# Kernel tuning notes

Measured on AMD Instinct MI355X. Metric: run time of the kernel, lower is better.

The kernel has to match this reference:

```python
import jax, jax.numpy as jnp
import numpy as np

N_NODES = 100000
N_EDGES = 1600000
N_GRAPHS = 256
IN_C = 64
HID = 128
OUT = 128
BN_EPS = 1e-5


def setup_inputs() -> dict:
    key = jax.random.key(0)
    ks = jax.random.split(key, 24)
    x = jax.random.normal(ks[0], (N_NODES, IN_C), jnp.float32)
    edge_index = jax.random.randint(ks[1], (2, N_EDGES), 0, N_NODES, dtype=jnp.int64 if jax.config.jax_enable_x64 else jnp.int32)
    batch = jnp.sort(jax.random.randint(ks[2], (N_NODES,), 0, N_GRAPHS))

    def lin(k, i, o):
        return (jax.random.normal(k, (i, o), jnp.float32) / np.float32(np.sqrt(i)))

    d = {"x": x, "edge_index": edge_index, "batch": batch}
    in_dims = [IN_C, HID, HID]
    for l in range(3):
        d[f"w1_{l}"] = lin(ks[3 + 6 * l], in_dims[l], HID)
        d[f"b1_{l}"] = jnp.zeros((HID,), jnp.float32)
        d[f"w2_{l}"] = lin(ks[4 + 6 * l], HID, HID)
        d[f"b2_{l}"] = jnp.zeros((HID,), jnp.float32)
        d[f"gamma_{l}"] = jnp.ones((HID,), jnp.float32)
        d[f"beta_{l}"] = jnp.zeros((HID,), jnp.float32)
    d["proj_w"] = lin(ks[22], HID, OUT)
    d["proj_b"] = jnp.zeros((OUT,), jnp.float32)
    return d


def _gin_forward(x, edge_index, batch, layers, proj_w, proj_b):
    src, dst = edge_index[0], edge_index[1]
    h = x
    for (w1, b1, w2, b2, g, b) in layers:
        # GINConv (eps=0, aggr='add'): MLP(h_i + sum_{j->i} h_j)
        agg = jax.ops.segment_sum(h[src], dst, num_segments=h.shape[0])
        z = h + agg
        z = jax.nn.relu(z @ w1 + b1) @ w2 + b2
        # BatchNorm1d, training mode (biased batch stats)
        mean = z.mean(axis=0)
        var = z.var(axis=0)
        z = (z - mean) * jax.lax.rsqrt(var + BN_EPS) * g + b
        h = jax.nn.relu(z)
    # global_mean_pool over graph ids
    s = jax.ops.segment_sum(h, batch, num_segments=N_GRAPHS)
    cnt = jax.ops.segment_sum(jnp.ones((h.shape[0], 1), h.dtype), batch, num_segments=N_GRAPHS)
    hg = s / jnp.maximum(cnt, 1.0)
    return hg @ proj_w + proj_b


def reference(x, edge_index, batch,
              w1_0, b1_0, w2_0, b2_0, gamma_0, beta_0,
              w1_1, b1_1, w2_1, b2_1, gamma_1, beta_1,
              w1_2, b1_2, w2_2, b2_2, gamma_2, beta_2,
              proj_w, proj_b):
    layers = [
        (w1_0, b1_0, w2_0, b2_0, gamma_0, beta_0),
        (w1_1, b1_1, w2_1, b2_1, gamma_1, beta_1),
        (w1_2, b1_2, w2_2, b2_2, gamma_2, beta_2),
    ]
    return _gin_forward(x, edge_index, batch, layers, proj_w, proj_b)
```

## Files before the change

kernel.cpp:

```cpp
#include <hip/hip_runtime.h>

#define N_NODES 100000
#define N_EDGES 1600000
#define N_GRAPHS 256
#define HID 128
#define BN_EPS 1e-5f

#define NT 1563
#define EB 4096
#define RB 391
#define MBLK 391
#define PB 3128

typedef __bf16 bf16x8 __attribute__((ext_vector_type(8)));
typedef __bf16 bf16x4 __attribute__((ext_vector_type(4)));
typedef __bf16 bf16x2 __attribute__((ext_vector_type(2)));
typedef float f32x4 __attribute__((ext_vector_type(4)));

__global__ __launch_bounds__(256) void setup_kernel(
    const float* __restrict__ x, __bf16* __restrict__ xb,
    const float* __restrict__ wa, const float* __restrict__ wb,
    const float* __restrict__ wc, const float* __restrict__ wd,
    const float* __restrict__ we, const float* __restrict__ wf,
    __bf16* __restrict__ wt,
    const int* __restrict__ batch, int* __restrict__ counts,
    const int* __restrict__ ei, int* __restrict__ tcnt) {
  __shared__ int hist[NT];
  int b = blockIdx.x;
  if (b < 6250) {
    int idx = b * 256 + threadIdx.x;
    if (idx >= N_NODES * 16) return;
    f32x4 v = ((const f32x4*)x)[idx];
    bf16x4 o = {(__bf16)v[0], (__bf16)v[1], (__bf16)v[2], (__bf16)v[3]};
    ((bf16x4*)xb)[idx] = o;
  } else if (b < 6250 + 352) {
    int idx = (b - 6250) * 256 + threadIdx.x;
    if (idx >= 90112) return;
    const float* w;
    int K, local;
    if (idx < 8192) { w = wa; K = 64; local = idx; }
    else {
      int s = (idx - 8192) / 16384;
      local = (idx - 8192) - s * 16384;
      K = 128;
      w = (s == 0) ? wb : (s == 1) ? wc : (s == 2) ? wd : (s == 3) ? we : wf;
    }
    int n = local / K, k = local - n * K;
    wt[idx] = (__bf16)w[k * 128 + n];
  } else if (b < 6609) {
    int t = (b - 6602) * 256 + threadIdx.x;
    int r0 = t * 64;
    if (r0 >= N_NODES) return;
    int rend = min(r0 + 64, N_NODES);
    int curg = batch[r0], cnt = 0;
    for (int r = r0; r < rend; r++) {
      int g = batch[r];
      if (g != curg) {
        atomicAdd(&counts[curg], cnt);
        curg = g;
        cnt = 1;
      } else {
        cnt++;
      }
    }
    atomicAdd(&counts[curg], cnt);
  } else {
    int t = threadIdx.x;
    for (int i = t; i < NT; i += 256) hist[i] = 0;
    __syncthreads();
    int base = (b - 6609) * EB;
#pragma unroll 4
    for (int i = 0; i < EB / 256; i++) {
      int e = base + i * 256 + t;
      if (e < N_EDGES) atomicAdd(&hist[ei[N_EDGES + e] >> 6], 1);
    }
    __syncthreads();
    for (int i = t; i < NT; i += 256) {
      int h = hist[i];
      if (h) atomicAdd(&tcnt[i], h);
    }
  }
}

__global__ __launch_bounds__(256) void tile_scan_kernel(const int* __restrict__ tcnt,
                                                        int* __restrict__ tstart,
                                                        int* __restrict__ gcursor) {
  __shared__ int ps[256];
  int t = threadIdx.x;
  const int CH = (NT + 255) / 256;
  int lo = t * CH, hi = min(lo + CH, NT);
  int s = 0;
  for (int i = lo; i < hi; i++) s += tcnt[i];
  ps[t] = s;
  __syncthreads();
  for (int off = 1; off < 256; off <<= 1) {
    int v = ps[t];
    int u = (t >= off) ? ps[t - off] : 0;
    __syncthreads();
    ps[t] = v + u;
    __syncthreads();
  }
  int base = (t == 0) ? 0 : ps[t - 1];
  for (int i = lo; i < hi; i++) {
    tstart[i] = base;
    gcursor[i] = base;
    base += tcnt[i];
  }
  if (t == 0) tstart[NT] = N_EDGES;
}

__global__ __launch_bounds__(256) void reorder2_kernel(const int* __restrict__ ei,
                                                       int* __restrict__ gcursor,
                                                       int* __restrict__ epack) {
  __shared__ int hist[NT];
  int t = threadIdx.x;
  for (int i = t; i < NT; i += 256) hist[i] = 0;
  __syncthreads();
  int base = blockIdx.x * EB;
#pragma unroll 4
  for (int i = 0; i < EB / 256; i++) {
    int e = base + i * 256 + t;
    if (e < N_EDGES) atomicAdd(&hist[ei[N_EDGES + e] >> 6], 1);
  }
  __syncthreads();
  for (int i = t; i < NT; i += 256) {
    int h = hist[i];
    if (h) hist[i] = atomicAdd(&gcursor[i], h);
  }
  __syncthreads();
#pragma unroll 4
  for (int i = 0; i < EB / 256; i++) {
    int e = base + i * 256 + t;
    if (e < N_EDGES) {
      int d = ei[N_EDGES + e];
      int s = ei[e];
      int pos = atomicAdd(&hist[d >> 6], 1);
      epack[pos] = (s << 6) | (d & 63);
    }
  }
}

__global__ __launch_bounds__(256) void row_sort_kernel(const int* __restrict__ tstart,
                                                       const int* __restrict__ epack,
                                                       int* __restrict__ starts,
                                                       int* __restrict__ srcs) {
  __shared__ int cnt[64];
  __shared__ int rbase[65];
  __shared__ int rofs[64];
  int t = threadIdx.x, b = blockIdx.x;
  int ts = tstart[b], te = tstart[b + 1];
  if (t < 64) cnt[t] = 0;
  __syncthreads();
  for (int i = ts + t; i < te; i += 256) atomicAdd(&cnt[epack[i] & 63], 1);
  __syncthreads();
  if (t == 0) {
    int a = 0;
    for (int r = 0; r < 64; r++) { rbase[r] = a; a += cnt[r]; }
    rbase[64] = a;
  }
  __syncthreads();
  if (t < 64) rofs[t] = ts + rbase[t];
  if (t <= 64) {
    int gr = b * 64 + t;
    if (gr <= N_NODES) starts[gr] = ts + rbase[t];
  }
  __syncthreads();
  for (int i = ts + t; i < te; i += 256) {
    int p = epack[i];
    int pos = atomicAdd(&rofs[p & 63], 1);
    srcs[pos] = p >> 6;
  }
}

template <int C, bool BN>
__global__ __launch_bounds__(256) void gather_kernel(const __bf16* __restrict__ h,
                                                     const float* __restrict__ accum,
                                                     const float* __restrict__ gamma,
                                                     const float* __restrict__ beta,
                                                     const int* __restrict__ starts,
                                                     const int* __restrict__ srcs,
                                                     __bf16* __restrict__ z) {
  const int lane = threadIdx.x & 63;
  const int row = __builtin_amdgcn_readfirstlane(blockIdx.x * 4 + (threadIdx.x >> 6));
  const int e0 = starts[row], e1 = starts[row + 1];

  if constexpr (C == 128) {
    float a0 = 0.f, a1 = 0.f, b0 = 0.f, b1 = 0.f;
    if constexpr (BN) {
      const int c0 = lane * 2, c1 = c0 + 1;
      const float invN = 1.f / (float)N_NODES;
      float m0 = accum[c0] * invN, m1 = accum[c1] * invN;
      float v0 = accum[HID + c0] * invN - m0 * m0;
      float v1 = accum[HID + c1] * invN - m1 * m1;
      a0 = gamma[c0] * rsqrtf(v0 + BN_EPS);
      a1 = gamma[c1] * rsqrtf(v1 + BN_EPS);
      b0 = beta[c0] - m0 * a0;
      b1 = beta[c1] - m1 * a1;
    }
#define ACCBN(vv, ss)                                                  \
    do {                                                               \
      if constexpr (BN) {                                              \
        ss.x += fmaxf(fmaf(a0, (float)(vv)[0], b0), 0.f);              \
        ss.y += fmaxf(fmaf(a1, (float)(vv)[1], b1), 0.f);              \
      } else {                                                         \
        ss.x += (float)(vv)[0];                                        \
        ss.y += (float)(vv)[1];                                        \
      }                                                                \
    } while (0)
    float2 s0 = {0.f, 0.f}, s1 = {0.f, 0.f}, s2 = {0.f, 0.f}, s3 = {0.f, 0.f};
    float2 s4 = {0.f, 0.f}, s5 = {0.f, 0.f}, s6 = {0.f, 0.f}, s7 = {0.f, 0.f};
    int e = e0;
    for (; e + 7 < e1; e += 8) {
      int i0 = srcs[e];
      int i1 = srcs[e + 1];
      int i2 = srcs[e + 2];
      int i3 = srcs[e + 3];
      int i4 = srcs[e + 4];
      int i5 = srcs[e + 5];
      int i6 = srcs[e + 6];
      int i7 = srcs[e + 7];
      bf16x2 v0 = *(const bf16x2*)(h + (size_t)i0 * 128 + lane * 2);
      bf16x2 v1 = *(const bf16x2*)(h + (size_t)i1 * 128 + lane * 2);
      bf16x2 v2 = *(const bf16x2*)(h + (size_t)i2 * 128 + lane * 2);
      bf16x2 v3 = *(const bf16x2*)(h + (size_t)i3 * 128 + lane * 2);
      bf16x2 v4 = *(const bf16x2*)(h + (size_t)i4 * 128 + lane * 2);
      bf16x2 v5 = *(const bf16x2*)(h + (size_t)i5 * 128 + lane * 2);
      bf16x2 v6 = *(const bf16x2*)(h + (size_t)i6 * 128 + lane * 2);
      bf16x2 v7 = *(const bf16x2*)(h + (size_t)i7 * 128 + lane * 2);
      ACCBN(v0, s0);
      ACCBN(v1, s1);
      ACCBN(v2, s2);
      ACCBN(v3, s3);
      ACCBN(v4, s4);
      ACCBN(v5, s5);
      ACCBN(v6, s6);
      ACCBN(v7, s7);
    }
    for (; e + 3 < e1; e += 4) {
      int i0 = srcs[e];
      int i1 = srcs[e + 1];
      int i2 = srcs[e + 2];
      int i3 = srcs[e + 3];
      bf16x2 v0 = *(const bf16x2*)(h + (size_t)i0 * 128 + lane * 2);
      bf16x2 v1 = *(const bf16x2*)(h + (size_t)i1 * 128 + lane * 2);
      bf16x2 v2 = *(const bf16x2*)(h + (size_t)i2 * 128 + lane * 2);
      bf16x2 v3 = *(const bf16x2*)(h + (size_t)i3 * 128 + lane * 2);
      ACCBN(v0, s0);
      ACCBN(v1, s1);
      ACCBN(v2, s2);
      ACCBN(v3, s3);
    }
    for (; e < e1; e++) {
      int i0 = srcs[e];
      bf16x2 vv = *(const bf16x2*)(h + (size_t)i0 * 128 + lane * 2);
      ACCBN(vv, s0);
    }
    bf16x2 sv = *(const bf16x2*)(h + (size_t)row * 128 + lane * 2);
    ACCBN(sv, s0);
    float tx = ((s0.x + s1.x) + (s2.x + s3.x)) + ((s4.x + s5.x) + (s6.x + s7.x));
    float ty = ((s0.y + s1.y) + (s2.y + s3.y)) + ((s4.y + s5.y) + (s6.y + s7.y));
    bf16x2 o = {(__bf16)tx, (__bf16)ty};
    *(bf16x2*)(z + (size_t)row * 128 + lane * 2) = o;
#undef ACCBN
  } else {
    float s0 = 0.f, s1 = 0.f, s2 = 0.f, s3 = 0.f;
    float s4 = 0.f, s5 = 0.f, s6 = 0.f, s7 = 0.f;
    int e = e0;
    for (; e + 7 < e1; e += 8) {
      int i0 = srcs[e];
      int i1 = srcs[e + 1];
      int i2 = srcs[e + 2];
      int i3 = srcs[e + 3];
      int i4 = srcs[e + 4];
      int i5 = srcs[e + 5];
      int i6 = srcs[e + 6];
      int i7 = srcs[e + 7];
      s0 += (float)h[(size_t)i0 * 64 + lane];
      s1 += (float)h[(size_t)i1 * 64 + lane];
      s2 += (float)h[(size_t)i2 * 64 + lane];
      s3 += (float)h[(size_t)i3 * 64 + lane];
      s4 += (float)h[(size_t)i4 * 64 + lane];
      s5 += (float)h[(size_t)i5 * 64 + lane];
      s6 += (float)h[(size_t)i6 * 64 + lane];
      s7 += (float)h[(size_t)i7 * 64 + lane];
    }
    for (; e + 3 < e1; e += 4) {
      int i0 = srcs[e];
      int i1 = srcs[e + 1];
      int i2 = srcs[e + 2];
      int i3 = srcs[e + 3];
      s0 += (float)h[(size_t)i0 * 64 + lane];
      s1 += (float)h[(size_t)i1 * 64 + lane];
      s2 += (float)h[(size_t)i2 * 64 + lane];
      s3 += (float)h[(size_t)i3 * 64 + lane];
    }
    for (; e < e1; e++) {
      int i0 = srcs[e];
      s0 += (float)h[(size_t)i0 * 64 + lane];
    }
    s0 += (float)h[(size_t)row * 64 + lane];
    float tot = ((s0 + s1) + (s2 + s3)) + ((s4 + s5) + (s6 + s7));
    z[(size_t)row * 64 + lane] = (__bf16)tot;
  }
}

template <int CIN>
__global__ __launch_bounds__(512, 1) void mlp_kernel(
    const __bf16* __restrict__ z, const __bf16* __restrict__ w1t,
    const float* __restrict__ b1, const __bf16* __restrict__ w2t,
    const float* __restrict__ b2, __bf16* __restrict__ u,
    float* __restrict__ part) {
  constexpr int CINP = CIN + 8;
  constexpr int TS = HID + 8;
  __shared__ __align__(16) __bf16 w1s[128 * CINP];
  __shared__ __align__(16) __bf16 w2s[128 * TS];
  __shared__ __align__(16) __bf16 hsm[8 * 16 * TS];

  const int tid = threadIdx.x;

  for (int i = tid; i < 128 * (CIN / 8); i += 512) {
    int r = i / (CIN / 8), c = i - r * (CIN / 8);
    *(bf16x8*)(w1s + r * CINP + c * 8) = *(const bf16x8*)(w1t + r * CIN + c * 8);
  }
  for (int i = tid; i < 128 * 16; i += 512) {
    int r = i >> 4, c = i & 15;
    *(bf16x8*)(w2s + r * TS + c * 8) = *(const bf16x8*)(w2t + r * HID + c * 8);
  }
  __syncthreads();

  const int wid = tid >> 6;
  const int lane = tid & 63;
  const int l16 = lane & 15;
  const int quad = lane >> 4;
  const int wgid = blockIdx.x * 8 + wid;
  const int rowbase = wgid * 32;
  const int nvalid = min(32, N_NODES - rowbase);
  __bf16* sm = hsm + wid * 16 * TS;

  if (nvalid <= 0) {
    float2 z2 = {0.f, 0.f};
    *(float2*)(part + (size_t)wgid * 256 + lane * 2) = z2;
    *(float2*)(part + (size_t)wgid * 256 + HID + lane * 2) = z2;
    return;
  }

  const f32x4 zero4 = {0.f, 0.f, 0.f, 0.f};
  float s0 = 0.f, q0 = 0.f, s1 = 0.f, q1 = 0.f;

#pragma unroll
  for (int m = 0; m < 2; m++) {
    const int mbase = rowbase + m * 16;
    const int nv_m = min(16, max(0, nvalid - m * 16));

    f32x4 acc[8];
#pragma unroll
    for (int ct = 0; ct < 8; ct++) acc[ct] = zero4;
#pragma unroll
    for (int ks = 0; ks < CIN / 32; ks++) {
      bf16x8 af = *(const bf16x8*)(z + (size_t)min(mbase + l16, N_NODES - 1) * CIN +
                                   ks * 32 + quad * 8);
#pragma unroll
      for (int ct = 0; ct < 8; ct++) {
        bf16x8 bfr = *(const bf16x8*)(w1s + (ct * 16 + l16) * CINP + ks * 32 + quad * 8);
        acc[ct] = __builtin_amdgcn_mfma_f32_16x16x32_bf16(af, bfr, acc[ct], 0, 0, 0);
      }
    }
#pragma unroll
    for (int ct = 0; ct < 8; ct++) {
      int col = ct * 16 + l16;
      float bias = b1[col];
#pragma unroll
      for (int r = 0; r < 4; r++) {
        float v = acc[ct][r] + bias;
        sm[(quad * 4 + r) * TS + col] = (__bf16)(v > 0.f ? v : 0.f);
      }
    }

#pragma unroll
    for (int ct = 0; ct < 8; ct++) acc[ct] = zero4;
#pragma unroll
    for (int ks = 0; ks < HID / 32; ks++) {
      bf16x8 af = *(const bf16x8*)(sm + l16 * TS + ks * 32 + quad * 8);
#pragma unroll
      for (int ct = 0; ct < 8; ct++) {
        bf16x8 bfr = *(const bf16x8*)(w2s + (ct * 16 + l16) * TS + ks * 32 + quad * 8);
        acc[ct] = __builtin_amdgcn_mfma_f32_16x16x32_bf16(af, bfr, acc[ct], 0, 0, 0);
      }
    }

#pragma unroll
    for (int ct = 0; ct < 8; ct++) {
      int col = ct * 16 + l16;
      float bias = b2[col];
#pragma unroll
      for (int r = 0; r < 4; r++)
        sm[(quad * 4 + r) * TS + col] = (__bf16)(acc[ct][r] + bias);
    }

    for (int f = lane; f < nv_m * 16; f += 64) {
      int r = f >> 4, c8 = f & 15;
      bf16x8 v = *(const bf16x8*)(sm + r * TS + c8 * 8);
      *(bf16x8*)(u + (size_t)(mbase + r) * HID + c8 * 8) = v;
    }

    for (int r = 0; r < nv_m; r++) {
      bf16x2 v = *(const bf16x2*)(sm + r * TS + lane * 2);
      float f0 = (float)v[0], f1 = (float)v[1];
      s0 += f0; q0 += f0 * f0;
      s1 += f1; q1 += f1 * f1;
    }
  }

  {
    float2 sp = {s0, s1}, qp = {q0, q1};
    *(float2*)(part + (size_t)wgid * 256 + lane * 2) = sp;
    *(float2*)(part + (size_t)wgid * 256 + HID + lane * 2) = qp;
  }
}

__global__ __launch_bounds__(256) void reduce_part_kernel(const float* __restrict__ part,
                                                          float* __restrict__ accum) {
  int t = threadIdx.x;
  float s = 0.f;
  for (int r = blockIdx.x; r < PB; r += gridDim.x)
    s += part[(size_t)r * 256 + t];
  atomicAdd(&accum[t], s);
}

__global__ __launch_bounds__(128) void bn_apply_pool_kernel(const __bf16* __restrict__ u,
                                                            const float* __restrict__ accum,
                                                            const float* __restrict__ gamma,
                                                            const float* __restrict__ beta,
                                                            const int* __restrict__ batch,
                                                            float* __restrict__ pool) {
  int c = threadIdx.x;
  int r0 = blockIdx.x * 64;
  if (r0 >= N_NODES) return;
  int rend = min(r0 + 64, N_NODES);
  const float invN = 1.f / (float)N_NODES;
  float mean = accum[c] * invN;
  float var = accum[HID + c] * invN - mean * mean;
  float a = gamma[c] * rsqrtf(var + BN_EPS);
  float b = beta[c] - mean * a;
  float accv = 0.f;
  int curg = -1;
  for (int r = r0; r < rend; r++) {
    int g = batch[r];
    if (g != curg) {
      if (curg >= 0) atomicAdd(&pool[curg * HID + c], accv);
      curg = g;
      accv = 0.f;
    }
    float v = (float)u[(size_t)r * HID + c];
    v = v * a + b;
    accv += (v > 0.f ? v : 0.f);
  }
  if (curg >= 0) atomicAdd(&pool[curg * HID + c], accv);
}

__global__ __launch_bounds__(128) void pool_proj_kernel(const float* __restrict__ pool,
                                                        const int* __restrict__ counts,
                                                        const float* __restrict__ pw,
                                                        const float* __restrict__ pb,
                                                        float* __restrict__ out) {
  int g = blockIdx.x;
  int c = threadIdx.x;
  __shared__ float hg[HID];
  float cnt = (float)max(counts[g], 1);
  hg[c] = pool[g * HID + c] / cnt;
  __syncthreads();
  float acc = pb[c];
#pragma unroll 8
  for (int k = 0; k < HID; k++) acc += hg[k] * pw[k * HID + c];
  out[g * HID + c] = acc;
}

extern "C" void kernel_launch(void* const* d_in, const int* in_sizes, int n_in,
                              void* d_out, int out_size, void* d_ws, size_t ws_size,
                              hipStream_t stream) {
  (void)in_sizes; (void)n_in; (void)out_size; (void)ws_size;
  const float* x = (const float*)d_in[0];
  const int* ei = (const int*)d_in[1];
  const int* batch = (const int*)d_in[2];
  const float* w1[3] = {(const float*)d_in[3], (const float*)d_in[9], (const float*)d_in[15]};
  const float* b1[3] = {(const float*)d_in[4], (const float*)d_in[10], (const float*)d_in[16]};
  const float* w2[3] = {(const float*)d_in[5], (const float*)d_in[11], (const float*)d_in[17]};
  const float* b2[3] = {(const float*)d_in[6], (const float*)d_in[12], (const float*)d_in[18]};
  const float* gm[3] = {(const float*)d_in[7], (const float*)d_in[13], (const float*)d_in[19]};
  const float* bt[3] = {(const float*)d_in[8], (const float*)d_in[14], (const float*)d_in[20]};
  const float* pw = (const float*)d_in[21];
  const float* pb = (const float*)d_in[22];
  float* out = (float*)d_out;

  char* ws = (char*)d_ws;
  __bf16* bufA = (__bf16*)ws;        ws += (size_t)N_NODES * HID * 2;
  __bf16* bufB = (__bf16*)ws;        ws += (size_t)N_NODES * HID * 2;
  __bf16* bufC = (__bf16*)ws;        ws += (size_t)N_NODES * HID * 2;
  __bf16* z0 = (__bf16*)ws;          ws += (size_t)N_NODES * 64 * 2;
  __bf16* xb = (__bf16*)ws;          ws += (size_t)N_NODES * 64 * 2;
  int* srcs = (int*)ws;              ws += (size_t)N_EDGES * 4;
  int* epack = (int*)ws;             ws += (size_t)N_EDGES * 4;
  int* starts = (int*)ws;            ws += (size_t)(N_NODES + 1) * 4;
  int* tcnt = (int*)ws;              ws += NT * 4;
  int* tstart = (int*)ws;            ws += (NT + 1) * 4;
  int* gcursor = (int*)ws;           ws += NT * 4;
  ws = (char*)(((uintptr_t)ws + 63) & ~(uintptr_t)63);
  float* part = (float*)ws;          ws += (size_t)PB * 256 * 4;
  __bf16* wt_all = (__bf16*)ws;      ws += 90112 * 2;
  ws = (char*)(((uintptr_t)ws + 63) & ~(uintptr_t)63);
  float* accum = (float*)ws;         ws += 3 * 256 * 4;
  float* pool = (float*)ws;          ws += N_GRAPHS * HID * 4;
  int* counts = (int*)ws;            ws += N_GRAPHS * 4;

  __bf16* w1t0 = wt_all;
  __bf16* w2t0 = wt_all + 8192;
  __bf16* w1t1 = wt_all + 24576;
  __bf16* w2t1 = wt_all + 40960;
  __bf16* w1t2 = wt_all + 57344;
  __bf16* w2t2 = wt_all + 73728;

  float* acc0 = accum;
  float* acc1 = accum + 256;
  float* acc2 = accum + 512;

  const int gat_blocks = (N_NODES + 3) / 4;

  hipMemsetAsync(accum, 0, 3 * 256 * 4 + (size_t)N_GRAPHS * HID * 4 + N_GRAPHS * 4, stream);
  hipMemsetAsync(tcnt, 0, NT * 4, stream);

  setup_kernel<<<7000, 256, 0, stream>>>(x, xb, w1[0], w2[0], w1[1], w2[1],
                                         w1[2], w2[2], wt_all, batch, counts, ei, tcnt);

  tile_scan_kernel<<<1, 256, 0, stream>>>(tcnt, tstart, gcursor);
  reorder2_kernel<<<RB, 256, 0, stream>>>(ei, gcursor, epack);
  row_sort_kernel<<<NT, 256, 0, stream>>>(tstart, epack, starts, srcs);

  gather_kernel<64, false><<<gat_blocks, 256, 0, stream>>>(xb, nullptr, nullptr, nullptr,
                                                           starts, srcs, z0);
  mlp_kernel<64><<<MBLK, 512, 0, stream>>>(z0, w1t0, b1[0], w2t0, b2[0], bufA, part);
  reduce_part_kernel<<<128, 256, 0, stream>>>(part, acc0);

  gather_kernel<128, true><<<gat_blocks, 256, 0, stream>>>(bufA, acc0, gm[0], bt[0],
                                                           starts, srcs, bufC);
  mlp_kernel<128><<<MBLK, 512, 0, stream>>>(bufC, w1t1, b1[1], w2t1, b2[1], bufB, part);
  reduce_part_kernel<<<128, 256, 0, stream>>>(part, acc1);

  gather_kernel<128, true><<<gat_blocks, 256, 0, stream>>>(bufB, acc1, gm[1], bt[1],
                                                           starts, srcs, bufC);
  mlp_kernel<128><<<MBLK, 512, 0, stream>>>(bufC, w1t2, b1[2], w2t2, b2[2], bufA, part);
  reduce_part_kernel<<<128, 256, 0, stream>>>(part, acc2);

  bn_apply_pool_kernel<<<NT, 128, 0, stream>>>(bufA, acc2, gm[2], bt[2], batch, pool);

  pool_proj_kernel<<<N_GRAPHS, 128, 0, stream>>>(pool, counts, pw, pb, out);
}
```

Measured before the change: 490.7 us.

## Split fused MLP kernel into two GEMM kernels with intermediate buffer

Replaces the fused two-layer MLP kernel (512 threads, one block per CU, large LDS) with two separate kernels: gemm1 writes the ReLU hidden activations to a global buffer and gemm2 reads them back, applies bias and computes BN partial statistics in registers with shuffle reductions. Each kernel uses smaller blocks with less LDS to raise occupancy. In exchange it adds an extra global write and read of a 100000x128 bf16 tensor per layer and an extra launch per layer. Row bounds checks are dropped because NW*32 exactly equals N_NODES.

```diff
diff --git a/kernel.cpp b/kernel.cpp
--- a/kernel.cpp
+++ b/kernel.cpp
@@ -9,7 +9,8 @@
 #define NT 1563
 #define EB 4096
 #define RB 391
-#define MBLK 391
+#define GB 782
+#define NW 3125
 #define PB 3128
 
 typedef __bf16 bf16x8 __attribute__((ext_vector_type(8)));
@@ -305,26 +306,16 @@
 }
 
 template <int CIN>
-__global__ __launch_bounds__(512, 1) void mlp_kernel(
+__global__ __launch_bounds__(256, 4) void gemm1_kernel(
     const __bf16* __restrict__ z, const __bf16* __restrict__ w1t,
-    const float* __restrict__ b1, const __bf16* __restrict__ w2t,
-    const float* __restrict__ b2, __bf16* __restrict__ u,
-    float* __restrict__ part) {
+    const float* __restrict__ b1, __bf16* __restrict__ t) {
   constexpr int CINP = CIN + 8;
-  constexpr int TS = HID + 8;
   __shared__ __align__(16) __bf16 w1s[128 * CINP];
-  __shared__ __align__(16) __bf16 w2s[128 * TS];
-  __shared__ __align__(16) __bf16 hsm[8 * 16 * TS];
 
   const int tid = threadIdx.x;
-
-  for (int i = tid; i < 128 * (CIN / 8); i += 512) {
+  for (int i = tid; i < 128 * (CIN / 8); i += 256) {
     int r = i / (CIN / 8), c = i - r * (CIN / 8);
     *(bf16x8*)(w1s + r * CINP + c * 8) = *(const bf16x8*)(w1t + r * CIN + c * 8);
-  }
-  for (int i = tid; i < 128 * 16; i += 512) {
-    int r = i >> 4, c = i & 15;
-    *(bf16x8*)(w2s + r * TS + c * 8) = *(const bf16x8*)(w2t + r * HID + c * 8);
   }
   __syncthreads();
 
@@ -332,89 +323,114 @@
   const int lane = tid & 63;
   const int l16 = lane & 15;
   const int quad = lane >> 4;
-  const int wgid = blockIdx.x * 8 + wid;
+  const int wgid = blockIdx.x * 4 + wid;
+  if (wgid >= NW) return;
   const int rowbase = wgid * 32;
-  const int nvalid = min(32, N_NODES - rowbase);
-  __bf16* sm = hsm + wid * 16 * TS;
-
-  if (nvalid <= 0) {
+
+  const f32x4 zero4 = {0.f, 0.f, 0.f, 0.f};
+#pragma unroll
+  for (int m = 0; m < 2; m++) {
+    const int mbase = rowbase + m * 16;
+    f32x4 acc[8];
+#pragma unroll
+    for (int ct = 0; ct < 8; ct++) acc[ct] = zero4;
+#pragma unroll
+    for (int ks = 0; ks < CIN / 32; ks++) {
+      bf16x8 af = *(const bf16x8*)(z + (size_t)(mbase + l16) * CIN + ks * 32 + quad * 8);
+#pragma unroll
+      for (int ct = 0; ct < 8; ct++) {
+        bf16x8 bfr = *(const bf16x8*)(w1s + (ct * 16 + l16) * CINP + ks * 32 + quad * 8);
+        acc[ct] = __builtin_amdgcn_mfma_f32_16x16x32_bf16(af, bfr, acc[ct], 0, 0, 0);
+      }
+    }
+#pragma unroll
+    for (int ct = 0; ct < 8; ct++) {
+      int col = ct * 16 + l16;
+      float bias = b1[col];
+#pragma unroll
+      for (int r = 0; r < 4; r++) {
+        float v = acc[ct][r] + bias;
+        t[(size_t)(mbase + quad * 4 + r) * HID + col] = (__bf16)(v > 0.f ? v : 0.f);
+      }
+    }
+  }
+}
+
+__global__ __launch_bounds__(256, 4) void gemm2_kernel(
+    const __bf16* __restrict__ t, const __bf16* __restrict__ w2t,
+    const float* __restrict__ b2, __bf16* __restrict__ u,
+    float* __restrict__ part) {
+  constexpr int TS = HID + 8;
+  __shared__ __align__(16) __bf16 w2s[128 * TS];
+
+  const int tid = threadIdx.x;
+  for (int i = tid; i < 128 * 16; i += 256) {
+    int r = i >> 4, c = i & 15;
+    *(bf16x8*)(w2s + r * TS + c * 8) = *(const bf16x8*)(w2t + r * HID + c * 8);
+  }
+  __syncthreads();
+
+  const int wid = tid >> 6;
+  const int lane = tid & 63;
+  const int l16 = lane & 15;
+  const int quad = lane >> 4;
+  const int wgid = blockIdx.x * 4 + wid;
+  if (wgid >= NW) {
     float2 z2 = {0.f, 0.f};
     *(float2*)(part + (size_t)wgid * 256 + lane * 2) = z2;
     *(float2*)(part + (size_t)wgid * 256 + HID + lane * 2) = z2;
     return;
   }
+  const int rowbase = wgid * 32;
 
   const f32x4 zero4 = {0.f, 0.f, 0.f, 0.f};
-  float s0 = 0.f, q0 = 0.f, s1 = 0.f, q1 = 0.f;
+  float cs[8], cq[8];
+#pragma unroll
+  for (int ct = 0; ct < 8; ct++) { cs[ct] = 0.f; cq[ct] = 0.f; }
 
 #pragma unroll
   for (int m = 0; m < 2; m++) {
     const int mbase = rowbase + m * 16;
-    const int nv_m = min(16, max(0, nvalid - m * 16));
-
     f32x4 acc[8];
 #pragma unroll
     for (int ct = 0; ct < 8; ct++) acc[ct] = zero4;
 #pragma unroll
-    for (int ks = 0; ks < CIN / 32; ks++) {
-      bf16x8 af = *(const bf16x8*)(z + (size_t)min(mbase + l16, N_NODES - 1) * CIN +
-                                   ks * 32 + quad * 8);
-#pragma unroll
-      for (int ct = 0; ct < 8; ct++) {
-        bf16x8 bfr = *(const bf16x8*)(w1s + (ct * 16 + l16) * CINP + ks * 32 + quad * 8);
-        acc[ct] = __builtin_amdgcn_mfma_f32_16x16x32_bf16(af, bfr, acc[ct], 0, 0, 0);
-      }
-    }
-#pragma unroll
-    for (int ct = 0; ct < 8; ct++) {
-      int col = ct * 16 + l16;
-      float bias = b1[col];
-#pragma unroll
-      for (int r = 0; r < 4; r++) {
-        float v = acc[ct][r] + bias;
-        sm[(quad * 4 + r) * TS + col] = (__bf16)(v > 0.f ? v : 0.f);
-      }
-    }
-
-#pragma unroll
-    for (int ct = 0; ct < 8; ct++) acc[ct] = zero4;
-#pragma unroll
     for (int ks = 0; ks < HID / 32; ks++) {
-      bf16x8 af = *(const bf16x8*)(sm + l16 * TS + ks * 32 + quad * 8);
+      bf16x8 af = *(const bf16x8*)(t + (size_t)(mbase + l16) * HID + ks * 32 + quad * 8);
 #pragma unroll
       for (int ct = 0; ct < 8; ct++) {
         bf16x8 bfr = *(const bf16x8*)(w2s + (ct * 16 + l16) * TS + ks * 32 + quad * 8);
         acc[ct] = __builtin_amdgcn_mfma_f32_16x16x32_bf16(af, bfr, acc[ct], 0, 0, 0);
       }
     }
-
 #pragma unroll
     for (int ct = 0; ct < 8; ct++) {
       int col = ct * 16 + l16;
       float bias = b2[col];
 #pragma unroll
-      for (int r = 0; r < 4; r++)
-        sm[(quad * 4 + r) * TS + col] = (__bf16)(acc[ct][r] + bias);
-    }
-
-    for (int f = lane; f < nv_m * 16; f += 64) {
-      int r = f >> 4, c8 = f & 15;
-      bf16x8 v = *(const bf16x8*)(sm + r * TS + c8 * 8);
-      *(bf16x8*)(u + (size_t)(mbase + r) * HID + c8 * 8) = v;
-    }
-
-    for (int r = 0; r < nv_m; r++) {
-      bf16x2 v = *(const bf16x2*)(sm + r * TS + lane * 2);
-      float f0 = (float)v[0], f1 = (float)v[1];
-      s0 += f0; q0 += f0 * f0;
-      s1 += f1; q1 += f1 * f1;
-    }
-  }
-
-  {
-    float2 sp = {s0, s1}, qp = {q0, q1};
-    *(float2*)(part + (size_t)wgid * 256 + lane * 2) = sp;
-    *(float2*)(part + (size_t)wgid * 256 + HID + lane * 2) = qp;
+      for (int r = 0; r < 4; r++) {
+        float v = acc[ct][r] + bias;
+        __bf16 bv = (__bf16)v;
+        u[(size_t)(mbase + quad * 4 + r) * HID + col] = bv;
+        float fv = (float)bv;
+        cs[ct] += fv;
+        cq[ct] += fv * fv;
+      }
+    }
+  }
+
+#pragma unroll
+  for (int ct = 0; ct < 8; ct++) {
+    float s = cs[ct];
+    s += __shfl_xor(s, 16);
+    s += __shfl_xor(s, 32);
+    float q = cq[ct];
+    q += __shfl_xor(q, 16);
+    q += __shfl_xor(q, 32);
+    if (quad == 0) {
+      part[(size_t)wgid * 256 + ct * 16 + l16] = s;
+      part[(size_t)wgid * 256 + HID + ct * 16 + l16] = q;
+    }
   }
 }
 
@@ -496,6 +512,7 @@
   __bf16* bufA = (__bf16*)ws;        ws += (size_t)N_NODES * HID * 2;
   __bf16* bufB = (__bf16*)ws;        ws += (size_t)N_NODES * HID * 2;
   __bf16* bufC = (__bf16*)ws;        ws += (size_t)N_NODES * HID * 2;
+  __bf16* tbuf = (__bf16*)ws;        ws += (size_t)N_NODES * HID * 2;
   __bf16* z0 = (__bf16*)ws;          ws += (size_t)N_NODES * 64 * 2;
   __bf16* xb = (__bf16*)ws;          ws += (size_t)N_NODES * 64 * 2;
   int* srcs = (int*)ws;              ws += (size_t)N_EDGES * 4;
@@ -537,17 +554,20 @@
 
   gather_kernel<64, false><<<gat_blocks, 256, 0, stream>>>(xb, nullptr, nullptr, nullptr,
                                                            starts, srcs, z0);
-  mlp_kernel<64><<<MBLK, 512, 0, stream>>>(z0, w1t0, b1[0], w2t0, b2[0], bufA, part);
+  gemm1_kernel<64><<<GB, 256, 0, stream>>>(z0, w1t0, b1[0], tbuf);
+  gemm2_kernel<<<GB, 256, 0, stream>>>(tbuf, w2t0, b2[0], bufA, part);
   reduce_part_kernel<<<128, 256, 0, stream>>>(part, acc0);
 
   gather_kernel<128, true><<<gat_blocks, 256, 0, stream>>>(bufA, acc0, gm[0], bt[0],
                                                            starts, srcs, bufC);
-  mlp_kernel<128><<<MBLK, 512, 0, stream>>>(bufC, w1t1, b1[1], w2t1, b2[1], bufB, part);
+  gemm1_kernel<128><<<GB, 256, 0, stream>>>(bufC, w1t1, b1[1], tbuf);
+  gemm2_kernel<<<GB, 256, 0, stream>>>(tbuf, w2t1, b2[1], bufB, part);
   reduce_part_kernel<<<128, 256, 0, stream>>>(part, acc1);
 
   gather_kernel<128, true><<<gat_blocks, 256, 0, stream>>>(bufB, acc1, gm[1], bt[1],
                                                            starts, srcs, bufC);
-  mlp_kernel<128><<<MBLK, 512, 0, stream>>>(bufC, w1t2, b1[2], w2t2, b2[2], bufA, part);
+  gemm1_kernel<128><<<GB, 256, 0, stream>>>(bufC, w1t2, b1[2], tbuf);
+  gemm2_kernel<<<GB, 256, 0, stream>>>(tbuf, w2t2, b2[2], bufA, part);
   reduce_part_kernel<<<128, 256, 0, stream>>>(part, acc2);
 
   bn_apply_pool_kernel<<<NT, 128, 0, stream>>>(bufA, acc2, gm[2], bt[2], batch, pool);
```

Result: slower. 510.4 us (+4.0%).
